# Kernel tuning notes

Measured on AMD Instinct MI355X. Metric: run time of the kernel, lower is better.

The kernel has to match this reference:

```python
import jax, jax.numpy as jnp
import numpy as np

N = 100000
E = 1600000
IN_C, HID_C, OUT_C = 64, 64, 40

def setup_inputs() -> dict:
    key = jax.random.key(0)
    ks = jax.random.split(key, 12)
    x = jax.random.normal(ks[0], (N, IN_C), dtype=jnp.float32)
    edge_index = jax.random.randint(ks[1], (2, E), 0, N, dtype=jnp.int32)
    def glorot(k, fan_in, fan_out):
        lim = float(np.sqrt(6.0 / (fan_in + fan_out)))
        return jax.random.uniform(k, (fan_in, fan_out), jnp.float32, -lim, lim)
    return {
        "x": x,
        "edge_index": edge_index,
        "W0_0": glorot(ks[2], IN_C, HID_C), "W1_0": glorot(ks[3], IN_C, HID_C), "b_0": jnp.zeros((HID_C,), jnp.float32),
        "W0_1": glorot(ks[4], HID_C, HID_C), "W1_1": glorot(ks[5], HID_C, HID_C), "b_1": jnp.zeros((HID_C,), jnp.float32),
        "W0_2": glorot(ks[6], HID_C, OUT_C), "W1_2": glorot(ks[7], HID_C, OUT_C), "b_2": jnp.zeros((OUT_C,), jnp.float32),
    }

def _cheb_norm(edge_index, num_nodes, dtype):
    # PyG ChebConv.__norm__ with normalization=None, edge_weight=None -> ones.
    # L = D - A; lambda_max = 2 * max(L weights); scaled: 2L/lambda_max - I.
    src, dst = edge_index[0], edge_index[1]
    w = jnp.ones((edge_index.shape[1],), dtype)
    deg = jax.ops.segment_sum(w, src, num_segments=num_nodes)
    lam = 2.0 * jnp.maximum(jnp.max(deg), jnp.max(-w))
    scale = 2.0 / lam
    norm_edge = -w * scale            # off-diagonal entries
    norm_loop = deg * scale - 1.0     # diagonal entries (self-loop mask subtracts 1)
    return norm_edge, norm_loop

def _spmm(x, src, dst, norm_edge, norm_loop, num_nodes):
    # y[i] = sum_{e: src->i} norm_e * x[src_e] + norm_loop[i] * x[i]
    msg = norm_edge[:, None] * x[src]
    return jax.ops.segment_sum(msg, dst, num_segments=num_nodes) + norm_loop[:, None] * x

def reference(x, edge_index, W0_0, W1_0, b_0, W0_1, W1_1, b_1, W0_2, W1_2, b_2):
    num_nodes = x.shape[0]
    src, dst = edge_index[0], edge_index[1]
    norm_edge, norm_loop = _cheb_norm(edge_index, num_nodes, x.dtype)

    def cheb(h, W0, W1, b):
        # K=2: out = T0(L) h W0 + T1(L) h W1 + b, T0 = I, T1 = scaled L
        Tx1 = _spmm(h, src, dst, norm_edge, norm_loop, num_nodes)
        return h @ W0 + Tx1 @ W1 + b

    h = jax.nn.relu(cheb(x, W0_0, W1_0, b_0))   # dropout is identity in eval mode
    h = jax.nn.relu(cheb(h, W0_1, W1_1, b_1))
    h = cheb(h, W0_2, W1_2, b_2)
    return jax.nn.log_softmax(h, axis=-1)
```

## Files before the change

kernel.cpp:

```cpp
#include <hip/hip_runtime.h>
#include <math.h>

#define N_NODES 100000
#define N_EDGES 1600000
#define OUTC 40
#define PAIRS40 20

#define NC 32
#define CHUNK (N_EDGES / NC)

#define RANGE_H 32768
#define NR_H 4
#define NPAD_H (NR_H * RANGE_H)

#define RANGE_F 16384
#define NR_F 7

#define FILLB (NC * NR_F)
#define NB32 (N_NODES / 32)
#define GEMB ((NB32 + 3) / 4)

#define SCAN_BLOCK 1024
#define SCAN_NBLK ((N_NODES + SCAN_BLOCK - 1) / SCAN_BLOCK)

typedef float vf2 __attribute__((ext_vector_type(2)));
typedef __fp16 f16x2 __attribute__((ext_vector_type(2)));

__device__ inline unsigned pack_bf16x2(float lo, float hi) {
    unsigned a = __float_as_uint(lo), b = __float_as_uint(hi);
    a = (a + 0x7fffu + ((a >> 16) & 1u)) >> 16;
    b = (b + 0x7fffu + ((b >> 16) & 1u)) & 0xffff0000u;
    return a | b;
}
__device__ inline float bf_lo(unsigned u) { return __uint_as_float(u << 16); }
__device__ inline float bf_hi(unsigned u) { return __uint_as_float(u & 0xffff0000u); }

__device__ inline unsigned pk16(float a, float b) {
    f16x2 h = __builtin_amdgcn_cvt_pkrtz(a, b);
    return __builtin_bit_cast(unsigned, h);
}
__device__ inline f16x2 uph(unsigned u) { return __builtin_bit_cast(f16x2, u); }

__device__ inline float fdot2(f16x2 a, f16x2 b, float c) {
#if __has_builtin(__builtin_amdgcn_fdot2)
    return __builtin_amdgcn_fdot2(a, b, c, false);
#else
    float d;
    asm volatile("v_dot2_f32_f16 %0, %1, %2, %3" : "=v"(d) : "v"(a), "v"(b), "v"(c));
    return d;
#endif
}

__global__ __launch_bounds__(1024) void k_hist(const int* __restrict__ src,
                                               const int* __restrict__ dst,
                                               unsigned short* __restrict__ Hs,
                                               unsigned short* __restrict__ Hd) {
    __shared__ unsigned h32[RANGE_H / 2];
    int c = blockIdx.x, r = blockIdx.y;
    const int* a = blockIdx.z ? dst : src;
    unsigned short* H = blockIdx.z ? Hd : Hs;
    for (int k = threadIdx.x; k < RANGE_H / 2; k += 1024) h32[k] = 0;
    __syncthreads();
    int r0 = r * RANGE_H;
    int e0 = c * CHUNK, e1 = e0 + CHUNK;
    for (int e = e0 + threadIdx.x; e < e1; e += 1024) {
        unsigned d = (unsigned)(a[e] - r0);
        if (d < RANGE_H) atomicAdd(&h32[d >> 1], 1u << ((d & 1) * 16));
    }
    __syncthreads();
    for (int k = threadIdx.x; k < RANGE_H; k += 1024)
        H[c * NPAD_H + r0 + k] = (unsigned short)((h32[k >> 1] >> ((k & 1) * 16)) & 0xffffu);
}

__global__ __launch_bounds__(SCAN_BLOCK) void k_scan1(const unsigned short* __restrict__ Hs,
                                                      const unsigned short* __restrict__ Hd,
                                                      int* __restrict__ rowptr,
                                                      int* __restrict__ blocksum,
                                                      int* __restrict__ deg_src,
                                                      int* __restrict__ maxdeg) {
    __shared__ int buf[2][SCAN_BLOCK];
    int t = threadIdx.x;
    int i = blockIdx.x * SCAN_BLOCK + t;
    int vs = 0, vd = 0;
    if (i < N_NODES) {
        #pragma unroll
        for (int c = 0; c < NC; c++) { vs += Hs[c * NPAD_H + i]; vd += Hd[c * NPAD_H + i]; }
        deg_src[i] = vs;
    }
    int m = vs;
    for (int off = 32; off; off >>= 1) m = max(m, __shfl_down(m, off));
    if ((t & 63) == 0) atomicMax(maxdeg, m);
    int pd = (vd + 7) & ~7;
    int cur = 0;
    buf[0][t] = pd;
    __syncthreads();
    for (int off = 1; off < SCAN_BLOCK; off <<= 1) {
        int nv = buf[cur][t];
        if (t >= off) nv += buf[cur][t - off];
        buf[1 - cur][t] = nv;
        cur = 1 - cur;
        __syncthreads();
    }
    int incl = buf[cur][t];
    if (i < N_NODES) rowptr[i + 1] = incl;
    if (t == SCAN_BLOCK - 1) blocksum[blockIdx.x] = incl;
}

__global__ __launch_bounds__(SCAN_BLOCK) void k_finalize(const int* __restrict__ blocksum,
                                                         int* __restrict__ rowptr,
                                                         const unsigned short* __restrict__ Hd,
                                                         int* __restrict__ Bd,
                                                         int* __restrict__ csr_src) {
    __shared__ int soff;
    int t = threadIdx.x, blk = blockIdx.x;
    if (t == 0) {
        int r = 0;
        for (int j = 0; j < blk; j++) r += blocksum[j];
        soff = r;
        if (blk == 0) rowptr[0] = 0;
    }
    __syncthreads();
    int i = blk * SCAN_BLOCK + t;
    if (i >= N_NODES) return;
    int tmp[NC];
    int s = 0;
    #pragma unroll
    for (int c = 0; c < NC; c++) { tmp[c] = Hd[c * NPAD_H + i]; s += tmp[c]; }
    int rf = rowptr[i + 1] + soff;
    rowptr[i + 1] = rf;
    int pd = (s + 7) & ~7;
    int run = rf - pd;
    #pragma unroll
    for (int c = 0; c < NC; c++) { Bd[c * NPAD_H + i] = run; run += tmp[c]; }
    for (int k = run; k < rf; k++) csr_src[k] = N_NODES;
}

__global__ __launch_bounds__(1024) void k_fill_gemm(const int* __restrict__ src,
                                                    const int* __restrict__ dst,
                                                    const int* __restrict__ basepos,
                                                    int* __restrict__ csr_src,
                                                    const float* __restrict__ hf,
                                                    const float* __restrict__ W0,
                                                    const float* __restrict__ W1,
                                                    const float* __restrict__ b,
                                                    const int* __restrict__ deg_src,
                                                    const int* __restrict__ maxdeg,
                                                    unsigned* __restrict__ G0b,
                                                    unsigned short* __restrict__ G1f8) {
    __shared__ union {
        int pos[RANGE_F];
        struct { uint4 swu[32 * 32]; unsigned shu[4 * 1024]; } g;
    } sm;
    int t = threadIdx.x;
    if (blockIdx.x < FILLB) {
        int c = blockIdx.x / NR_F, r = blockIdx.x % NR_F;
        int r0 = r * RANGE_F;
        for (int k = t; k < RANGE_F; k += 1024) sm.pos[k] = basepos[c * NPAD_H + r0 + k];
        __syncthreads();
        int e0 = c * CHUNK, e1 = e0 + CHUNK;
        for (int e = e0 + t; e < e1; e += 1024) {
            unsigned d = (unsigned)(dst[e] - r0);
            if (d < RANGE_F) {
                int s = src[e];
                int p = atomicAdd(&sm.pos[d], 1);
                csr_src[p] = s;
            }
        }
        return;
    }
    int gb = blockIdx.x - FILLB;
    int sub = t >> 8, tt = t & 255;
    int nb = gb * 4 + sub;
    bool ok = nb < NB32;
    const float2* W02 = (const float2*)W0;
    const float2* W12 = (const float2*)W1;
    {
        int kp = t >> 5, c2 = t & 31;
        float2 a  = W02[(kp * 2) * 32 + c2];
        float2 bb = W02[(kp * 2 + 1) * 32 + c2];
        float2 cc = W12[(kp * 2) * 32 + c2];
        float2 dd = W12[(kp * 2 + 1) * 32 + c2];
        sm.g.swu[t] = make_uint4(pk16(a.x, bb.x), pk16(a.y, bb.y), pk16(cc.x, dd.x), pk16(cc.y, dd.y));
    }
    if (ok) {
        const float4* h4 = (const float4*)(hf + (size_t)(nb * 32) * 64);
        float4 f0 = h4[tt * 2], f1 = h4[tt * 2 + 1];
        ((uint4*)(sm.g.shu + sub * 1024))[tt] =
            make_uint4(pk16(f0.x, f0.y), pk16(f0.z, f0.w), pk16(f1.x, f1.y), pk16(f1.z, f1.w));
    }
    if (blockIdx.x == FILLB && t < 16) ((unsigned*)G1f8)[N_NODES * 16 + t] = 0;
    __syncthreads();
    if (!ok) return;
    int c2 = tt & 31, rg = tt >> 5;
    int i0 = nb * 32;
    const unsigned* shu = sm.g.shu + sub * 1024;
    float scale = 1.0f / (float)(*maxdeg);
    float2 b2 = ((const float2*)b)[c2];
    float a0x[4], a0y[4], a1x[4], a1y[4];
    #pragma unroll
    for (int p = 0; p < 4; p++) { a0x[p] = b2.x; a0y[p] = b2.y; a1x[p] = 0.f; a1y[p] = 0.f; }
    #pragma unroll 8
    for (int kp = 0; kp < 32; kp++) {
        uint4 w = sm.g.swu[kp * 32 + c2];
        f16x2 w0x = uph(w.x), w0y = uph(w.y), w1x = uph(w.z), w1y = uph(w.w);
        #pragma unroll
        for (int p = 0; p < 4; p++) {
            f16x2 h2 = uph(shu[(rg + 8 * p) * 32 + kp]);
            a0x[p] = fdot2(h2, w0x, a0x[p]);
            a0y[p] = fdot2(h2, w0y, a0y[p]);
            a1x[p] = fdot2(h2, w1x, a1x[p]);
            a1y[p] = fdot2(h2, w1y, a1y[p]);
        }
    }
    #pragma unroll
    for (int p = 0; p < 4; p++) {
        int row = i0 + rg + 8 * p;
        float nl = (float)deg_src[row] * scale - 1.0f;
        G0b[row * 32 + c2] = pack_bf16x2(a0x[p] + nl * a1x[p], a0y[p] + nl * a1y[p]);
        int pk = __builtin_amdgcn_cvt_pk_fp8_f32(a1x[p], a1y[p], 0, false);
        G1f8[row * 32 + c2] = (unsigned short)(pk & 0xffff);
    }
}

__global__ __launch_bounds__(256, 6) void k_fs64_g64(const unsigned* __restrict__ G0b_in,
                                                     const unsigned char* __restrict__ g1_in,
                                                     const int* __restrict__ rowptr,
                                                     const int* __restrict__ csr_src,
                                                     const int* __restrict__ deg_src,
                                                     const int* __restrict__ maxdeg,
                                                     const float* __restrict__ W0,
                                                     const float* __restrict__ W1,
                                                     const float* __restrict__ b,
                                                     unsigned* __restrict__ G0b_out,
                                                     unsigned short* __restrict__ G1f8_out) {
    __shared__ uint4 swu[32 * 32];
    __shared__ unsigned shu[32 * 32];
    int t = threadIdx.x;
    const float2* W02 = (const float2*)W0;
    const float2* W12 = (const float2*)W1;
    for (int cell = t; cell < 1024; cell += 256) {
        int kp = cell >> 5, c2 = cell & 31;
        float2 a  = W02[(kp * 2) * 32 + c2];
        float2 bb = W02[(kp * 2 + 1) * 32 + c2];
        float2 cc = W12[(kp * 2) * 32 + c2];
        float2 dd = W12[(kp * 2 + 1) * 32 + c2];
        swu[cell] = make_uint4(pk16(a.x, bb.x), pk16(a.y, bb.y), pk16(cc.x, dd.x), pk16(cc.y, dd.y));
    }
    int waveId = t >> 6, lane = t & 63;
    int ch = lane & 7;
    int local = waveId * 8 + (lane >> 3);
    int node = blockIdx.x * 32 + local;
    float scale = 1.0f / (float)(*maxdeg);
    int e0 = rowptr[node], e1 = rowptr[node + 1];
    int octbase = lane & 56;
    vf2 acc[4];
    acc[0] = 0.f; acc[1] = 0.f; acc[2] = 0.f; acc[3] = 0.f;
    uint2 u[8];
    int idxB = 0;
    int e = e0;
    if (e < e1) {
        int idxA = csr_src[e + ch];
        if (e + 8 < e1) idxB = csr_src[e + 8 + ch];
        #pragma unroll
        for (int j = 0; j < 8; j++) {
            int s = __shfl(idxA, octbase | j);
            u[j] = ((const uint2*)(g1_in + (size_t)s * 64))[ch];
        }
    }
    while (e < e1) {
        int en = e + 8;
        int idxC = 0;
        if (en + 8 < e1) idxC = csr_src[en + 8 + ch];
        uint2 n[8];
        if (en < e1) {
            #pragma unroll
            for (int j = 0; j < 8; j++) {
                int s = __shfl(idxB, octbase | j);
                n[j] = ((const uint2*)(g1_in + (size_t)s * 64))[ch];
            }
        }
        #pragma unroll
        for (int j = 0; j < 8; j++) {
            acc[0] += __builtin_amdgcn_cvt_pk_f32_fp8((int)u[j].x, false);
            acc[1] += __builtin_amdgcn_cvt_pk_f32_fp8((int)u[j].x, true);
            acc[2] += __builtin_amdgcn_cvt_pk_f32_fp8((int)u[j].y, false);
            acc[3] += __builtin_amdgcn_cvt_pk_f32_fp8((int)u[j].y, true);
        }
        #pragma unroll
        for (int j = 0; j < 8; j++) u[j] = n[j];
        idxB = idxC;
        e = en;
    }
    uint4 g = ((const uint4*)(G0b_in + (size_t)node * 32))[ch];
    float v0 = fmaxf(bf_lo(g.x) - scale * acc[0].x, 0.f);
    float v1 = fmaxf(bf_hi(g.x) - scale * acc[0].y, 0.f);
    float v2 = fmaxf(bf_lo(g.y) - scale * acc[1].x, 0.f);
    float v3 = fmaxf(bf_hi(g.y) - scale * acc[1].y, 0.f);
    float v4 = fmaxf(bf_lo(g.z) - scale * acc[2].x, 0.f);
    float v5 = fmaxf(bf_hi(g.z) - scale * acc[2].y, 0.f);
    float v6 = fmaxf(bf_lo(g.w) - scale * acc[3].x, 0.f);
    float v7 = fmaxf(bf_hi(g.w) - scale * acc[3].y, 0.f);
    ((uint4*)shu)[local * 8 + ch] = make_uint4(pk16(v0, v1), pk16(v2, v3), pk16(v4, v5), pk16(v6, v7));
    if (blockIdx.x == 0 && t < 16) ((unsigned*)G1f8_out)[N_NODES * 16 + t] = 0;
    __syncthreads();
    int c2 = t & 31, rg = t >> 5;
    int i0 = blockIdx.x * 32;
    float2 b2 = ((const float2*)b)[c2];
    float a0x[4], a0y[4], a1x[4], a1y[4];
    #pragma unroll
    for (int p = 0; p < 4; p++) { a0x[p] = b2.x; a0y[p] = b2.y; a1x[p] = 0.f; a1y[p] = 0.f; }
    #pragma unroll 8
    for (int kp = 0; kp < 32; kp++) {
        uint4 w = swu[kp * 32 + c2];
        f16x2 w0x = uph(w.x), w0y = uph(w.y), w1x = uph(w.z), w1y = uph(w.w);
        #pragma unroll
        for (int p = 0; p < 4; p++) {
            f16x2 h2 = uph(shu[(rg + 8 * p) * 32 + kp]);
            a0x[p] = fdot2(h2, w0x, a0x[p]);
            a0y[p] = fdot2(h2, w0y, a0y[p]);
            a1x[p] = fdot2(h2, w1x, a1x[p]);
            a1y[p] = fdot2(h2, w1y, a1y[p]);
        }
    }
    #pragma unroll
    for (int p = 0; p < 4; p++) {
        int row = i0 + rg + 8 * p;
        float nl = (float)deg_src[row] * scale - 1.0f;
        G0b_out[row * 32 + c2] = pack_bf16x2(a0x[p] + nl * a1x[p], a0y[p] + nl * a1y[p]);
        int pk = __builtin_amdgcn_cvt_pk_fp8_f32(a1x[p], a1y[p], 0, false);
        G1f8_out[row * 32 + c2] = (unsigned short)(pk & 0xffff);
    }
}

__global__ __launch_bounds__(256, 6) void k_fs64_g40(const unsigned* __restrict__ G0b_in,
                                                     const unsigned char* __restrict__ g1_in,
                                                     const int* __restrict__ rowptr,
                                                     const int* __restrict__ csr_src,
                                                     const int* __restrict__ deg_src,
                                                     const int* __restrict__ maxdeg,
                                                     const float* __restrict__ W0,
                                                     const float* __restrict__ W1,
                                                     const float* __restrict__ b,
                                                     unsigned* __restrict__ G0b_out,
                                                     unsigned short* __restrict__ G1f8_out) {
    __shared__ uint4 swu[32 * PAIRS40];
    __shared__ unsigned shu[32 * 32];
    int t = threadIdx.x;
    const float2* W02 = (const float2*)W0;
    const float2* W12 = (const float2*)W1;
    for (int cell = t; cell < 32 * PAIRS40; cell += 256) {
        int kp = cell / PAIRS40, c2 = cell % PAIRS40;
        float2 a  = W02[(kp * 2) * PAIRS40 + c2];
        float2 bb = W02[(kp * 2 + 1) * PAIRS40 + c2];
        float2 cc = W12[(kp * 2) * PAIRS40 + c2];
        float2 dd = W12[(kp * 2 + 1) * PAIRS40 + c2];
        swu[cell] = make_uint4(pk16(a.x, bb.x), pk16(a.y, bb.y), pk16(cc.x, dd.x), pk16(cc.y, dd.y));
    }
    int waveId = t >> 6, lane = t & 63;
    int ch = lane & 7;
    int local = waveId * 8 + (lane >> 3);
    int node = blockIdx.x * 32 + local;
    float scale = 1.0f / (float)(*maxdeg);
    int e0 = rowptr[node], e1 = rowptr[node + 1];
    int octbase = lane & 56;
    vf2 acc[4];
    acc[0] = 0.f; acc[1] = 0.f; acc[2] = 0.f; acc[3] = 0.f;
    uint2 u[8];
    int idxB = 0;
    int e = e0;
    if (e < e1) {
        int idxA = csr_src[e + ch];
        if (e + 8 < e1) idxB = csr_src[e + 8 + ch];
        #pragma unroll
        for (int j = 0; j < 8; j++) {
            int s = __shfl(idxA, octbase | j);
            u[j] = ((const uint2*)(g1_in + (size_t)s * 64))[ch];
        }
    }
    while (e < e1) {
        int en = e + 8;
        int idxC = 0;
        if (en + 8 < e1) idxC = csr_src[en + 8 + ch];
        uint2 n[8];
        if (en < e1) {
            #pragma unroll
            for (int j = 0; j < 8; j++) {
                int s = __shfl(idxB, octbase | j);
                n[j] = ((const uint2*)(g1_in + (size_t)s * 64))[ch];
            }
        }
        #pragma unroll
        for (int j = 0; j < 8; j++) {
            acc[0] += __builtin_amdgcn_cvt_pk_f32_fp8((int)u[j].x, false);
            acc[1] += __builtin_amdgcn_cvt_pk_f32_fp8((int)u[j].x, true);
            acc[2] += __builtin_amdgcn_cvt_pk_f32_fp8((int)u[j].y, false);
            acc[3] += __builtin_amdgcn_cvt_pk_f32_fp8((int)u[j].y, true);
        }
        #pragma unroll
        for (int j = 0; j < 8; j++) u[j] = n[j];
        idxB = idxC;
        e = en;
    }
    uint4 g = ((const uint4*)(G0b_in + (size_t)node * 32))[ch];
    float v0 = fmaxf(bf_lo(g.x) - scale * acc[0].x, 0.f);
    float v1 = fmaxf(bf_hi(g.x) - scale * acc[0].y, 0.f);
    float v2 = fmaxf(bf_lo(g.y) - scale * acc[1].x, 0.f);
    float v3 = fmaxf(bf_hi(g.y) - scale * acc[1].y, 0.f);
    float v4 = fmaxf(bf_lo(g.z) - scale * acc[2].x, 0.f);
    float v5 = fmaxf(bf_hi(g.z) - scale * acc[2].y, 0.f);
    float v6 = fmaxf(bf_lo(g.w) - scale * acc[3].x, 0.f);
    float v7 = fmaxf(bf_hi(g.w) - scale * acc[3].y, 0.f);
    ((uint4*)shu)[local * 8 + ch] = make_uint4(pk16(v0, v1), pk16(v2, v3), pk16(v4, v5), pk16(v6, v7));
    if (blockIdx.x == 0 && t < 10) ((unsigned*)G1f8_out)[N_NODES * 10 + t] = 0;
    __syncthreads();
    int c2 = t & 31, rg = t >> 5;
    if (c2 >= PAIRS40) return;
    int i0 = blockIdx.x * 32;
    float2 b2 = ((const float2*)b)[c2];
    float a0x[4], a0y[4], a1x[4], a1y[4];
    #pragma unroll
    for (int p = 0; p < 4; p++) { a0x[p] = b2.x; a0y[p] = b2.y; a1x[p] = 0.f; a1y[p] = 0.f; }
    #pragma unroll 8
    for (int kp = 0; kp < 32; kp++) {
        uint4 w = swu[kp * PAIRS40 + c2];
        f16x2 w0x = uph(w.x), w0y = uph(w.y), w1x = uph(w.z), w1y = uph(w.w);
        #pragma unroll
        for (int p = 0; p < 4; p++) {
            f16x2 h2 = uph(shu[(rg + 8 * p) * 32 + kp]);
            a0x[p] = fdot2(h2, w0x, a0x[p]);
            a0y[p] = fdot2(h2, w0y, a0y[p]);
            a1x[p] = fdot2(h2, w1x, a1x[p]);
            a1y[p] = fdot2(h2, w1y, a1y[p]);
        }
    }
    #pragma unroll
    for (int p = 0; p < 4; p++) {
        int row = i0 + rg + 8 * p;
        float nl = (float)deg_src[row] * scale - 1.0f;
        G0b_out[row * PAIRS40 + c2] = pack_bf16x2(a0x[p] + nl * a1x[p], a0y[p] + nl * a1y[p]);
        int pk = __builtin_amdgcn_cvt_pk_fp8_f32(a1x[p], a1y[p], 0, false);
        G1f8_out[row * PAIRS40 + c2] = (unsigned short)(pk & 0xffff);
    }
}

__global__ __launch_bounds__(256, 6) void k_spmm40(const unsigned* __restrict__ G0b,
                                                   const unsigned char* __restrict__ g1,
                                                   const int* __restrict__ rowptr,
                                                   const int* __restrict__ csr_src,
                                                   const int* __restrict__ maxdeg,
                                                   float* __restrict__ out) {
    int t = threadIdx.x;
    int waveId = t >> 6, lane = t & 63;
    int ch = lane & 7;
    bool act = ch < 5;
    int node = blockIdx.x * 32 + waveId * 8 + (lane >> 3);
    float scale = 1.0f / (float)(*maxdeg);
    int e0 = rowptr[node], e1 = rowptr[node + 1];
    int octbase = lane & 56;
    vf2 acc[4];
    acc[0] = 0.f; acc[1] = 0.f; acc[2] = 0.f; acc[3] = 0.f;
    uint2 u[8];
    int idxB = 0;
    int e = e0;
    if (e < e1) {
        int idxA = csr_src[e + ch];
        if (e + 8 < e1) idxB = csr_src[e + 8 + ch];
        #pragma unroll
        for (int j = 0; j < 8; j++) {
            int s = __shfl(idxA, octbase | j);
            if (act) u[j] = ((const uint2*)(g1 + (size_t)s * 40))[ch];
        }
    }
    while (e < e1) {
        int en = e + 8;
        int idxC = 0;
        if (en + 8 < e1) idxC = csr_src[en + 8 + ch];
        uint2 n[8];
        if (en < e1) {
            #pragma unroll
            for (int j = 0; j < 8; j++) {
                int s = __shfl(idxB, octbase | j);
                if (act) n[j] = ((const uint2*)(g1 + (size_t)s * 40))[ch];
            }
        }
        if (act) {
            #pragma unroll
            for (int j = 0; j < 8; j++) {
                acc[0] += __builtin_amdgcn_cvt_pk_f32_fp8((int)u[j].x, false);
                acc[1] += __builtin_amdgcn_cvt_pk_f32_fp8((int)u[j].x, true);
                acc[2] += __builtin_amdgcn_cvt_pk_f32_fp8((int)u[j].y, false);
                acc[3] += __builtin_amdgcn_cvt_pk_f32_fp8((int)u[j].y, true);
            }
        }
        #pragma unroll
        for (int j = 0; j < 8; j++) u[j] = n[j];
        idxB = idxC;
        e = en;
    }
    float v[8];
    float m = -INFINITY;
    if (act) {
        uint4 g = ((const uint4*)(G0b + (size_t)node * PAIRS40))[ch];
        v[0] = bf_lo(g.x) - scale * acc[0].x;
        v[1] = bf_hi(g.x) - scale * acc[0].y;
        v[2] = bf_lo(g.y) - scale * acc[1].x;
        v[3] = bf_hi(g.y) - scale * acc[1].y;
        v[4] = bf_lo(g.z) - scale * acc[2].x;
        v[5] = bf_hi(g.z) - scale * acc[2].y;
        v[6] = bf_lo(g.w) - scale * acc[3].x;
        v[7] = bf_hi(g.w) - scale * acc[3].y;
        #pragma unroll
        for (int q = 0; q < 8; q++) m = fmaxf(m, v[q]);
    }
    m = fmaxf(m, __shfl_xor(m, 1));
    m = fmaxf(m, __shfl_xor(m, 2));
    m = fmaxf(m, __shfl_xor(m, 4));
    float s = 0.f;
    if (act) {
        #pragma unroll
        for (int q = 0; q < 8; q++) s += __expf(v[q] - m);
    }
    s += __shfl_xor(s, 1);
    s += __shfl_xor(s, 2);
    s += __shfl_xor(s, 4);
    float ls = __logf(s);
    if (act) {
        float4 oA, oB;
        oA.x = v[0] - m - ls; oA.y = v[1] - m - ls; oA.z = v[2] - m - ls; oA.w = v[3] - m - ls;
        oB.x = v[4] - m - ls; oB.y = v[5] - m - ls; oB.z = v[6] - m - ls; oB.w = v[7] - m - ls;
        float4* o4 = (float4*)(out + (size_t)node * 40);
        o4[ch * 2] = oA;
        o4[ch * 2 + 1] = oB;
    }
}


extern "C" void kernel_launch(void* const* d_in, const int* in_sizes, int n_in,
                              void* d_out, int out_size, void* d_ws, size_t ws_size,
                              hipStream_t stream) {
    const float* x   = (const float*)d_in[0];
    const int* ei    = (const int*)d_in[1];
    const int* src   = ei;
    const int* dst   = ei + N_EDGES;
    const float* W0_0 = (const float*)d_in[2];
    const float* W1_0 = (const float*)d_in[3];
    const float* b_0  = (const float*)d_in[4];
    const float* W0_1 = (const float*)d_in[5];
    const float* W1_1 = (const float*)d_in[6];
    const float* b_1  = (const float*)d_in[7];
    const float* W0_2 = (const float*)d_in[8];
    const float* W1_2 = (const float*)d_in[9];
    const float* b_2  = (const float*)d_in[10];
    float* outp = (float*)d_out;

    int* ip = (int*)d_ws;
    int* deg_src  = ip;
    int* rowptr   = ip + 100000;
    int* blocksum = ip + 200064;
    int* maxdeg   = ip + 200192;
    int* csr_src  = ip + 200256;
    unsigned short* Hs = (unsigned short*)(ip + 2700256);
    unsigned short* Hd = (unsigned short*)(ip + 4797408);
    int* Bd       = ip + 6894560;
    unsigned* GA0 = (unsigned*)(ip + 11088864);
    unsigned short* GA1 = (unsigned short*)(ip + 14288864);
    unsigned* GB0 = (unsigned*)(ip + 15888928);
    unsigned short* GB1 = (unsigned short*)(ip + 19088928);

    (void)hipMemsetAsync(maxdeg, 0, sizeof(int), stream);

    k_hist<<<dim3(NC, NR_H, 2), 1024, 0, stream>>>(src, dst, Hs, Hd);
    k_scan1<<<SCAN_NBLK, SCAN_BLOCK, 0, stream>>>(Hs, Hd, rowptr, blocksum, deg_src, maxdeg);
    k_finalize<<<SCAN_NBLK, SCAN_BLOCK, 0, stream>>>(blocksum, rowptr, Hd, Bd, csr_src);

    k_fill_gemm<<<FILLB + GEMB, 1024, 0, stream>>>(src, dst, Bd, csr_src,
                                                   x, W0_0, W1_0, b_0, deg_src, maxdeg, GA0, GA1);

    const int GS = N_NODES / 32;

    k_fs64_g64<<<GS, 256, 0, stream>>>(GA0, (const unsigned char*)GA1, rowptr, csr_src,
                                       deg_src, maxdeg, W0_1, W1_1, b_1, GB0, GB1);
    k_fs64_g40<<<GS, 256, 0, stream>>>(GB0, (const unsigned char*)GB1, rowptr, csr_src,
                                       deg_src, maxdeg, W0_2, W1_2, b_2, GA0, GA1);
    k_spmm40<<<GS, 256, 0, stream>>>(GA0, (const unsigned char*)GA1, rowptr, csr_src, maxdeg, outp);
}
```

Baseline: 301.4 us.

## Vectorize shared-memory H reads in GEMM loops and raise occupancy bounds

The dense GEMM inner loops now read four k-pairs of the H row at once as a uint4 from shared memory, fully unroll the k loop and issue four weight loads per step. This cuts the number of LDS instructions in the fused gather and GEMM kernels. Launch bounds for the SpMM/GEMM kernels rise from 6 to 8 waves per SIMD, which squeezes register allocation. The fill-block index mapping is also changed so consecutive blocks take different edge chunks within the same node range.

```diff
diff --git a/kernel.cpp b/kernel.cpp
--- a/kernel.cpp
+++ b/kernel.cpp
@@ -50,6 +50,27 @@
     return d;
 #endif
 }
+
+#define DOT2_KP4(hq, w0_, w1_, w2_, w3_, p)                                  \
+    {                                                                        \
+        f16x2 h0 = uph((hq).x), h1 = uph((hq).y), h2 = uph((hq).z), h3 = uph((hq).w); \
+        a0x[p] = fdot2(h0, uph((w0_).x), a0x[p]);                            \
+        a0y[p] = fdot2(h0, uph((w0_).y), a0y[p]);                            \
+        a1x[p] = fdot2(h0, uph((w0_).z), a1x[p]);                            \
+        a1y[p] = fdot2(h0, uph((w0_).w), a1y[p]);                            \
+        a0x[p] = fdot2(h1, uph((w1_).x), a0x[p]);                            \
+        a0y[p] = fdot2(h1, uph((w1_).y), a0y[p]);                            \
+        a1x[p] = fdot2(h1, uph((w1_).z), a1x[p]);                            \
+        a1y[p] = fdot2(h1, uph((w1_).w), a1y[p]);                            \
+        a0x[p] = fdot2(h2, uph((w2_).x), a0x[p]);                            \
+        a0y[p] = fdot2(h2, uph((w2_).y), a0y[p]);                            \
+        a1x[p] = fdot2(h2, uph((w2_).z), a1x[p]);                            \
+        a1y[p] = fdot2(h2, uph((w2_).w), a1y[p]);                            \
+        a0x[p] = fdot2(h3, uph((w3_).x), a0x[p]);                            \
+        a0y[p] = fdot2(h3, uph((w3_).y), a0y[p]);                            \
+        a1x[p] = fdot2(h3, uph((w3_).z), a1x[p]);                            \
+        a1y[p] = fdot2(h3, uph((w3_).w), a1y[p]);                            \
+    }
 
 __global__ __launch_bounds__(1024) void k_hist(const int* __restrict__ src,
                                                const int* __restrict__ dst,
@@ -153,7 +174,7 @@
     } sm;
     int t = threadIdx.x;
     if (blockIdx.x < FILLB) {
-        int c = blockIdx.x / NR_F, r = blockIdx.x % NR_F;
+        int c = blockIdx.x & 31, r = blockIdx.x >> 5;
         int r0 = r * RANGE_F;
         for (int k = t; k < RANGE_F; k += 1024) sm.pos[k] = basepos[c * NPAD_H + r0 + k];
         __syncthreads();
@@ -199,17 +220,16 @@
     float a0x[4], a0y[4], a1x[4], a1y[4];
     #pragma unroll
     for (int p = 0; p < 4; p++) { a0x[p] = b2.x; a0y[p] = b2.y; a1x[p] = 0.f; a1y[p] = 0.f; }
-    #pragma unroll 8
-    for (int kp = 0; kp < 32; kp++) {
-        uint4 w = sm.g.swu[kp * 32 + c2];
-        f16x2 w0x = uph(w.x), w0y = uph(w.y), w1x = uph(w.z), w1y = uph(w.w);
+    #pragma unroll
+    for (int kp4 = 0; kp4 < 32; kp4 += 4) {
+        uint4 w0 = sm.g.swu[(kp4 + 0) * 32 + c2];
+        uint4 w1 = sm.g.swu[(kp4 + 1) * 32 + c2];
+        uint4 w2 = sm.g.swu[(kp4 + 2) * 32 + c2];
+        uint4 w3 = sm.g.swu[(kp4 + 3) * 32 + c2];
         #pragma unroll
         for (int p = 0; p < 4; p++) {
-            f16x2 h2 = uph(shu[(rg + 8 * p) * 32 + kp]);
-            a0x[p] = fdot2(h2, w0x, a0x[p]);
-            a0y[p] = fdot2(h2, w0y, a0y[p]);
-            a1x[p] = fdot2(h2, w1x, a1x[p]);
-            a1y[p] = fdot2(h2, w1y, a1y[p]);
+            uint4 hq = ((const uint4*)(shu + (rg + 8 * p) * 32))[kp4 >> 2];
+            DOT2_KP4(hq, w0, w1, w2, w3, p);
         }
     }
     #pragma unroll
@@ -222,7 +242,7 @@
     }
 }
 
-__global__ __launch_bounds__(256, 6) void k_fs64_g64(const unsigned* __restrict__ G0b_in,
+__global__ __launch_bounds__(256, 8) void k_fs64_g64(const unsigned* __restrict__ G0b_in,
                                                      const unsigned char* __restrict__ g1_in,
                                                      const int* __restrict__ rowptr,
                                                      const int* __restrict__ csr_src,
@@ -309,17 +329,16 @@
     float a0x[4], a0y[4], a1x[4], a1y[4];
     #pragma unroll
     for (int p = 0; p < 4; p++) { a0x[p] = b2.x; a0y[p] = b2.y; a1x[p] = 0.f; a1y[p] = 0.f; }
-    #pragma unroll 8
-    for (int kp = 0; kp < 32; kp++) {
-        uint4 w = swu[kp * 32 + c2];
-        f16x2 w0x = uph(w.x), w0y = uph(w.y), w1x = uph(w.z), w1y = uph(w.w);
+    #pragma unroll
+    for (int kp4 = 0; kp4 < 32; kp4 += 4) {
+        uint4 w0 = swu[(kp4 + 0) * 32 + c2];
+        uint4 w1 = swu[(kp4 + 1) * 32 + c2];
+        uint4 w2 = swu[(kp4 + 2) * 32 + c2];
+        uint4 w3 = swu[(kp4 + 3) * 32 + c2];
         #pragma unroll
         for (int p = 0; p < 4; p++) {
-            f16x2 h2 = uph(shu[(rg + 8 * p) * 32 + kp]);
-            a0x[p] = fdot2(h2, w0x, a0x[p]);
-            a0y[p] = fdot2(h2, w0y, a0y[p]);
-            a1x[p] = fdot2(h2, w1x, a1x[p]);
-            a1y[p] = fdot2(h2, w1y, a1y[p]);
+            uint4 hq = ((const uint4*)(shu + (rg + 8 * p) * 32))[kp4 >> 2];
+            DOT2_KP4(hq, w0, w1, w2, w3, p);
         }
     }
     #pragma unroll
@@ -332,7 +351,7 @@
     }
 }
 
-__global__ __launch_bounds__(256, 6) void k_fs64_g40(const unsigned* __restrict__ G0b_in,
+__global__ __launch_bounds__(256, 8) void k_fs64_g40(const unsigned* __restrict__ G0b_in,
                                                      const unsigned char* __restrict__ g1_in,
                                                      const int* __restrict__ rowptr,
                                                      const int* __restrict__ csr_src,
@@ -420,17 +439,16 @@
     float a0x[4], a0y[4], a1x[4], a1y[4];
     #pragma unroll
     for (int p = 0; p < 4; p++) { a0x[p] = b2.x; a0y[p] = b2.y; a1x[p] = 0.f; a1y[p] = 0.f; }
-    #pragma unroll 8
-    for (int kp = 0; kp < 32; kp++) {
-        uint4 w = swu[kp * PAIRS40 + c2];
-        f16x2 w0x = uph(w.x), w0y = uph(w.y), w1x = uph(w.z), w1y = uph(w.w);
+    #pragma unroll
+    for (int kp4 = 0; kp4 < 32; kp4 += 4) {
+        uint4 w0 = swu[(kp4 + 0) * PAIRS40 + c2];
+        uint4 w1 = swu[(kp4 + 1) * PAIRS40 + c2];
+        uint4 w2 = swu[(kp4 + 2) * PAIRS40 + c2];
+        uint4 w3 = swu[(kp4 + 3) * PAIRS40 + c2];
         #pragma unroll
         for (int p = 0; p < 4; p++) {
-            f16x2 h2 = uph(shu[(rg + 8 * p) * 32 + kp]);
-            a0x[p] = fdot2(h2, w0x, a0x[p]);
-            a0y[p] = fdot2(h2, w0y, a0y[p]);
-            a1x[p] = fdot2(h2, w1x, a1x[p]);
-            a1y[p] = fdot2(h2, w1y, a1y[p]);
+            uint4 hq = ((const uint4*)(shu + (rg + 8 * p) * 32))[kp4 >> 2];
+            DOT2_KP4(hq, w0, w1, w2, w3, p);
         }
     }
     #pragma unroll
@@ -443,7 +461,7 @@
     }
 }
 
-__global__ __launch_bounds__(256, 6) void k_spmm40(const unsigned* __restrict__ G0b,
+__global__ __launch_bounds__(256, 8) void k_spmm40(const unsigned* __restrict__ G0b,
                                                    const unsigned char* __restrict__ g1,
                                                    const int* __restrict__ rowptr,
                                                    const int* __restrict__ csr_src,
```

Result: no change. 296.9 us (-1.5%).
